# Kernel tuning notes

Measured on AMD Instinct MI355X. Metric: run time of the kernel, lower is better.

The kernel has to match this reference:

```python
import jax, jax.numpy as jnp
import numpy as np

NUM_CLASSES = 101
BATCH = 262144
LAMBDA = 1000.0


def setup_inputs() -> dict:
    key = jax.random.key(0)
    k1, k2 = jax.random.split(key)
    outputs = jax.random.normal(k1, (BATCH, NUM_CLASSES), dtype=jnp.float32)
    targets = jax.random.randint(k2, (BATCH,), 0, NUM_CLASSES, dtype=jnp.int64)
    return {"outputs": outputs, "targets": targets}


def reference(outputs, targets):
    B, C = outputs.shape
    targets = targets.reshape(-1)
    tf = targets.astype(outputs.dtype)

    probs = jax.nn.softmax(outputs, axis=1)                      # [B, C]
    labels = jnp.arange(C, dtype=outputs.dtype)                  # [C]
    pred_values = jnp.sum(probs * labels[None, :], axis=1)       # [B]
    centered = labels[None, :] - pred_values[:, None]            # [B, C]
    variance = jnp.sum(probs * centered * centered, axis=1)      # [B]
    variance = jnp.clip(variance, 1e-6, None)
    est_err = (pred_values - tf) ** 2
    concentrated_loss = jnp.mean(0.5 * jnp.log(variance) + est_err / (2.0 * variance))

    # Unimodal ordinal penalty, vectorized over the original double loop:
    # sign_j = -1 if j < target else +1; penalty = relu(-(p_j - p_{j+1}) * sign_j)
    j = jnp.arange(C - 1)                                        # [C-1]
    sign = jnp.where(j[None, :] < targets[:, None], -1.0, 1.0).astype(outputs.dtype)
    prob_diff = probs[:, :-1] - probs[:, 1:]                     # [B, C-1]
    penalty = jax.nn.relu(-prob_diff * sign)
    unimodal_loss = jnp.sum(penalty) / B
    weighted_unimodal_loss = LAMBDA * unimodal_loss

    total_loss = concentrated_loss + weighted_unimodal_loss
    return (total_loss, concentrated_loss, weighted_unimodal_loss)
```

## Files before the change

### kernel.cpp

```cpp
#include <hip/hip_runtime.h>
#include <hip/hip_bf16.h>


#define ROWS_PER_BLOCK 128
#define NCLASSES 101
#define LAMBDA_W 1000.0

__global__ __launch_bounds__(ROWS_PER_BLOCK)
void ucl_row_kernel(const float* __restrict__ x,
                    const int* __restrict__ tgt,
                    double* __restrict__ acc)
{
    __shared__ float lds[ROWS_PER_BLOCK * NCLASSES];

    const int tid = threadIdx.x;
    const int bid = blockIdx.x;

    {
        const float4* __restrict__ g4 =
            reinterpret_cast<const float4*>(x + (size_t)bid * (ROWS_PER_BLOCK * NCLASSES));
        float4* __restrict__ l4 = reinterpret_cast<float4*>(lds);
#pragma unroll
        for (int k = 0; k < 25; ++k)
            l4[tid + 128 * k] = g4[tid + 128 * k];
        if (tid < 32)
            l4[tid + 3200] = g4[tid + 3200];
    }
    __syncthreads();

    const float* __restrict__ xr = lds + tid * NCLASSES;
    const int t = tgt[(size_t)bid * ROWS_PER_BLOCK + tid];

    float S, W, Q, pen, eprev;
    {
        float e = __expf(xr[0]);
        S = e; W = 0.0f; Q = 0.0f; pen = 0.0f; eprev = e;
    }
#pragma unroll
    for (int j = 1; j < NCLASSES; ++j) {
        float e  = __expf(xr[j]);
        float fj = (float)j;
        S += e;
        W  = fmaf(e, fj, W);
        Q  = fmaf(e, fj * fj, Q);
        float d = eprev - e;
        float r = ((j - 1) < t) ? d : -d;
        pen += fmaxf(r, 0.0f);
        eprev = e;
    }

    const float pred = W / S;
    float var = fmaf(-pred, pred, Q / S);
    var = fmaxf(var, 1e-6f);
    const float err  = pred - (float)t;
    float conc = 0.5f * __logf(var) + err * err / (2.0f * var);
    float pens = pen / S;

#pragma unroll
    for (int off = 32; off > 0; off >>= 1) {
        conc += __shfl_down(conc, off);
        pens += __shfl_down(pens, off);
    }
    __syncthreads();
    if ((tid & 63) == 0) {
        lds[(tid >> 6) * 2 + 0] = conc;
        lds[(tid >> 6) * 2 + 1] = pens;
    }
    __syncthreads();
    if (tid == 0) {
        double c = (double)lds[0] + (double)lds[2];
        double p = (double)lds[1] + (double)lds[3];
        atomicAdd(&acc[0], c);
        atomicAdd(&acc[1], p);
    }
}

__global__ void ucl_finalize_kernel(const double* __restrict__ acc,
                                    float* __restrict__ out,
                                    double invB)
{
    double conc = acc[0] * invB;
    double uni  = acc[1] * invB * LAMBDA_W;
    out[0] = (float)(conc + uni);
    out[1] = (float)conc;
    out[2] = (float)uni;
}

extern "C" void kernel_launch(void* const* d_in, const int* in_sizes, int n_in,
                              void* d_out, int out_size, void* d_ws, size_t ws_size,
                              hipStream_t stream)
{
    const float* x   = (const float*)d_in[0];
    const int*   tgt = (const int*)d_in[1];
    float* out  = (float*)d_out;
    double* acc = (double*)d_ws;

    const int B = in_sizes[1];
    const int blocks = B / ROWS_PER_BLOCK;

    hipMemsetAsync(d_ws, 0, 2 * sizeof(double), stream);
    hipLaunchKernelGGL(ucl_row_kernel, dim3(blocks), dim3(ROWS_PER_BLOCK), 0, stream,
                       x, tgt, acc);
    hipLaunchKernelGGL(ucl_finalize_kernel, dim3(1), dim3(1), 0, stream,
                       acc, out, 1.0 / (double)B);
}
```

Before: 189.0 us.

## Split each row across two threads and replace atomics with per-block partials

Each block now uses 256 threads for 128 rows. The two halves of the class dimension are processed by separate threads and merged through shared memory, which doubles the parallelism available per row and shortens the serial exp chain. The global load is reorganized to issue all loads into registers before storing to LDS. When enough workspace is available, double atomics are replaced by per-block float2 partials summed in a tree-reducing finalize kernel, which also removes the memset. The cost is an extra barrier and some LDS traffic.

New measurement: 157.4 us. -16.7%, faster.

```diff
diff --git a/kernel.cpp b/kernel.cpp
--- a/kernel.cpp
+++ b/kernel.cpp
@@ -1,89 +1,156 @@
 #include <hip/hip_runtime.h>
-#include <hip/hip_bf16.h>
 
 
-#define ROWS_PER_BLOCK 128
-#define NCLASSES 101
+#define NR 128
+#define NT 256
+#define NC 101
 #define LAMBDA_W 1000.0
 
-__global__ __launch_bounds__(ROWS_PER_BLOCK)
+__global__ __launch_bounds__(NT, 3)
 void ucl_row_kernel(const float* __restrict__ x,
                     const int* __restrict__ tgt,
-                    double* __restrict__ acc)
+                    float2* __restrict__ partial,
+                    double* __restrict__ acc,
+                    int use_atomic)
 {
-    __shared__ float lds[ROWS_PER_BLOCK * NCLASSES];
+    __shared__ float tile[NR * NC];
+    __shared__ float part[NR * 4];
+    __shared__ float red[8];
 
     const int tid = threadIdx.x;
     const int bid = blockIdx.x;
 
     {
         const float4* __restrict__ g4 =
-            reinterpret_cast<const float4*>(x + (size_t)bid * (ROWS_PER_BLOCK * NCLASSES));
-        float4* __restrict__ l4 = reinterpret_cast<float4*>(lds);
+            reinterpret_cast<const float4*>(x + (size_t)bid * (NR * NC));
+        float4* __restrict__ l4 = reinterpret_cast<float4*>(tile);
+        float4 v[12]; float4 vt;
 #pragma unroll
-        for (int k = 0; k < 25; ++k)
-            l4[tid + 128 * k] = g4[tid + 128 * k];
-        if (tid < 32)
-            l4[tid + 3200] = g4[tid + 3200];
+        for (int k = 0; k < 12; ++k) v[k] = g4[tid + NT * k];
+        if (tid < 160) vt = g4[3072 + tid];
+#pragma unroll
+        for (int k = 0; k < 12; ++k) l4[tid + NT * k] = v[k];
+        if (tid < 160) l4[3072 + tid] = vt;
+    }
+
+    const int row = tid & (NR - 1);
+    const int t = tgt[(size_t)bid * NR + row];
+    __syncthreads();
+
+    const float* __restrict__ xr = tile + row * NC;
+    float S, W, Q, pen;
+    if (tid < NR) {
+        float e = __expf(xr[0]);
+        S = e; W = 0.f; Q = 0.f; pen = 0.f;
+        float eprev = e;
+#pragma unroll
+        for (int j = 1; j <= 50; ++j) {
+            float e2 = __expf(xr[j]);
+            float fj = (float)j;
+            S += e2;
+            W = fmaf(e2, fj, W);
+            Q = fmaf(e2, fj * fj, Q);
+            float d = eprev - e2;
+            float r = ((j - 1) < t) ? d : -d;
+            pen += fmaxf(r, 0.f);
+            eprev = e2;
+        }
+    } else {
+        float eprev = __expf(xr[50]);
+        S = 0.f; W = 0.f; Q = 0.f; pen = 0.f;
+#pragma unroll
+        for (int j = 51; j < NC; ++j) {
+            float e2 = __expf(xr[j]);
+            float fj = (float)j;
+            S += e2;
+            W = fmaf(e2, fj, W);
+            Q = fmaf(e2, fj * fj, Q);
+            float d = eprev - e2;
+            float r = ((j - 1) < t) ? d : -d;
+            pen += fmaxf(r, 0.f);
+            eprev = e2;
+        }
+        part[row * 4 + 0] = S;
+        part[row * 4 + 1] = W;
+        part[row * 4 + 2] = Q;
+        part[row * 4 + 3] = pen;
     }
     __syncthreads();
 
-    const float* __restrict__ xr = lds + tid * NCLASSES;
-    const int t = tgt[(size_t)bid * ROWS_PER_BLOCK + tid];
-
-    float S, W, Q, pen, eprev;
-    {
-        float e = __expf(xr[0]);
-        S = e; W = 0.0f; Q = 0.0f; pen = 0.0f; eprev = e;
+    float conc = 0.f, pens = 0.f;
+    if (tid < NR) {
+        S   += part[row * 4 + 0];
+        W   += part[row * 4 + 1];
+        Q   += part[row * 4 + 2];
+        pen += part[row * 4 + 3];
+        float pred = W / S;
+        float var = fmaf(-pred, pred, Q / S);
+        var = fmaxf(var, 1e-6f);
+        float err = pred - (float)t;
+        conc = 0.5f * __logf(var) + err * err / (2.0f * var);
+        pens = pen / S;
     }
-#pragma unroll
-    for (int j = 1; j < NCLASSES; ++j) {
-        float e  = __expf(xr[j]);
-        float fj = (float)j;
-        S += e;
-        W  = fmaf(e, fj, W);
-        Q  = fmaf(e, fj * fj, Q);
-        float d = eprev - e;
-        float r = ((j - 1) < t) ? d : -d;
-        pen += fmaxf(r, 0.0f);
-        eprev = e;
-    }
-
-    const float pred = W / S;
-    float var = fmaf(-pred, pred, Q / S);
-    var = fmaxf(var, 1e-6f);
-    const float err  = pred - (float)t;
-    float conc = 0.5f * __logf(var) + err * err / (2.0f * var);
-    float pens = pen / S;
 
 #pragma unroll
     for (int off = 32; off > 0; off >>= 1) {
         conc += __shfl_down(conc, off);
         pens += __shfl_down(pens, off);
     }
-    __syncthreads();
     if ((tid & 63) == 0) {
-        lds[(tid >> 6) * 2 + 0] = conc;
-        lds[(tid >> 6) * 2 + 1] = pens;
+        red[(tid >> 6) * 2 + 0] = conc;
+        red[(tid >> 6) * 2 + 1] = pens;
     }
     __syncthreads();
     if (tid == 0) {
-        double c = (double)lds[0] + (double)lds[2];
-        double p = (double)lds[1] + (double)lds[3];
-        atomicAdd(&acc[0], c);
-        atomicAdd(&acc[1], p);
+        float c = red[0] + red[2] + red[4] + red[6];
+        float p = red[1] + red[3] + red[5] + red[7];
+        if (use_atomic) {
+            atomicAdd(&acc[0], (double)c);
+            atomicAdd(&acc[1], (double)p);
+        } else {
+            partial[bid] = make_float2(c, p);
+        }
     }
 }
 
-__global__ void ucl_finalize_kernel(const double* __restrict__ acc,
-                                    float* __restrict__ out,
-                                    double invB)
+__global__ __launch_bounds__(256)
+void ucl_finalize(const float2* __restrict__ partial,
+                  const double* __restrict__ acc,
+                  float* __restrict__ out,
+                  int nblocks, double invB, int use_atomic)
 {
-    double conc = acc[0] * invB;
-    double uni  = acc[1] * invB * LAMBDA_W;
-    out[0] = (float)(conc + uni);
-    out[1] = (float)conc;
-    out[2] = (float)uni;
+    const int tid = threadIdx.x;
+    if (use_atomic) {
+        if (tid == 0) {
+            double C = acc[0] * invB;
+            double P = acc[1] * invB * LAMBDA_W;
+            out[0] = (float)(C + P);
+            out[1] = (float)C;
+            out[2] = (float)P;
+        }
+        return;
+    }
+    double c = 0.0, p = 0.0;
+    for (int i = tid; i < nblocks; i += 256) {
+        float2 v = partial[i];
+        c += (double)v.x;
+        p += (double)v.y;
+    }
+#pragma unroll
+    for (int off = 32; off > 0; off >>= 1) {
+        c += __shfl_down(c, off);
+        p += __shfl_down(p, off);
+    }
+    __shared__ double s[8];
+    if ((tid & 63) == 0) { s[(tid >> 6) * 2] = c; s[(tid >> 6) * 2 + 1] = p; }
+    __syncthreads();
+    if (tid == 0) {
+        double C = (s[0] + s[2] + s[4] + s[6]) * invB;
+        double P = (s[1] + s[3] + s[5] + s[7]) * invB * LAMBDA_W;
+        out[0] = (float)(C + P);
+        out[1] = (float)C;
+        out[2] = (float)P;
+    }
 }
 
 extern "C" void kernel_launch(void* const* d_in, const int* in_sizes, int n_in,
@@ -92,15 +159,21 @@
 {
     const float* x   = (const float*)d_in[0];
     const int*   tgt = (const int*)d_in[1];
-    float* out  = (float*)d_out;
+    float* out = (float*)d_out;
+
+    const int B = in_sizes[1];
+    const int blocks = B / NR;
+
+    const size_t need = (size_t)blocks * sizeof(float2);
+    const int use_atomic = (ws_size < need + 2 * sizeof(double)) ? 1 : 0;
+    float2* partial = (float2*)((char*)d_ws + 2 * sizeof(double));
     double* acc = (double*)d_ws;
 
-    const int B = in_sizes[1];
-    const int blocks = B / ROWS_PER_BLOCK;
+    if (use_atomic)
+        hipMemsetAsync(d_ws, 0, 2 * sizeof(double), stream);
 
-    hipMemsetAsync(d_ws, 0, 2 * sizeof(double), stream);
-    hipLaunchKernelGGL(ucl_row_kernel, dim3(blocks), dim3(ROWS_PER_BLOCK), 0, stream,
-                       x, tgt, acc);
-    hipLaunchKernelGGL(ucl_finalize_kernel, dim3(1), dim3(1), 0, stream,
-                       acc, out, 1.0 / (double)B);
+    hipLaunchKernelGGL(ucl_row_kernel, dim3(blocks), dim3(NT), 0, stream,
+                       x, tgt, partial, acc, use_atomic);
+    hipLaunchKernelGGL(ucl_finalize, dim3(1), dim3(256), 0, stream,
+                       partial, acc, out, blocks, 1.0 / (double)B, use_atomic);
 }
```

## Persistent double-buffered row kernel with async global-to-LDS loads and partial sums

Applied to the files above, without the earlier changes.

Turns the row kernel into a persistent kernel. At most 512 blocks each walk a contiguous range of 128-row tiles, and the next tile is prefetched into a second LDS buffer with global_load_lds while the current tile is computed. The double-precision atomics and the memset are replaced by per-block float2 partials, which a 256-thread finalize kernel reduces in double. The aim is to hide global load latency behind the exp/accumulate work and to drop the atomic and memset overhead. In exchange, the two ~52KB LDS buffers limit each CU to one 2-wave block, and correctness depends on the compiler's wait counts covering the async LDS writes.

New measurement: 173.9 us. 8.0% less time.

```diff
diff --git a/kernel.cpp b/kernel.cpp
--- a/kernel.cpp
+++ b/kernel.cpp
@@ -1,89 +1,132 @@
 #include <hip/hip_runtime.h>
-#include <hip/hip_bf16.h>
 
 
-#define ROWS_PER_BLOCK 128
-#define NCLASSES 101
+#define NT 128
+#define TR 128
+#define NC 101
+#define TILE_F4 3232
+#define PAD_F4 3328
+#define NBLK 512
 #define LAMBDA_W 1000.0
 
-__global__ __launch_bounds__(ROWS_PER_BLOCK)
+__device__ __forceinline__ void gload_lds16(const float4* g, float4* l)
+{
+    __builtin_amdgcn_global_load_lds(
+        (const __attribute__((address_space(1))) void*)g,
+        (__attribute__((address_space(3))) void*)l,
+        16, 0, 0);
+}
+
+__device__ __forceinline__ void prefetch_tile(const float4* __restrict__ g4,
+                                              float4* l4, int tid)
+{
+#pragma unroll
+    for (int k = 0; k < 25; ++k)
+        gload_lds16(g4 + k * NT + tid, l4 + k * NT + tid);
+    if (tid < 32)
+        gload_lds16(g4 + 25 * NT + tid, l4 + 25 * NT + tid);
+}
+
+__global__ __launch_bounds__(NT)
 void ucl_row_kernel(const float* __restrict__ x,
                     const int* __restrict__ tgt,
-                    double* __restrict__ acc)
+                    float2* __restrict__ partial,
+                    int ntiles)
 {
-    __shared__ float lds[ROWS_PER_BLOCK * NCLASSES];
+    __shared__ __align__(16) float4 buf[2][PAD_F4];
+    __shared__ float red[4];
 
     const int tid = threadIdx.x;
     const int bid = blockIdx.x;
+    const int nb  = gridDim.x;
 
-    {
-        const float4* __restrict__ g4 =
-            reinterpret_cast<const float4*>(x + (size_t)bid * (ROWS_PER_BLOCK * NCLASSES));
-        float4* __restrict__ l4 = reinterpret_cast<float4*>(lds);
+    const int tpb   = ntiles / nb;
+    const int rem   = ntiles - tpb * nb;
+    const int start = bid * tpb + (bid < rem ? bid : rem);
+    const int cnt   = tpb + (bid < rem ? 1 : 0);
+
+    const float4* __restrict__ x4 = (const float4*)x;
+
+    int t_cur = tgt[(size_t)start * TR + tid];
+    prefetch_tile(x4 + (size_t)start * TILE_F4, buf[0], tid);
+
+    float conc = 0.f, pens = 0.f;
+
+    for (int i = 0; i < cnt; ++i) {
+        __syncthreads();
+
+        if (i + 1 < cnt)
+            prefetch_tile(x4 + (size_t)(start + i + 1) * TILE_F4,
+                          buf[(i + 1) & 1], tid);
+        int t_next = (i + 1 < cnt) ? tgt[(size_t)(start + i + 1) * TR + tid] : 0;
+
+        const float* __restrict__ xr = (const float*)buf[i & 1] + tid * NC;
+        const int t = t_cur;
+
+        float e = __expf(xr[0]);
+        float S = e, W = 0.f, Q = 0.f, pen = 0.f, ep = e;
 #pragma unroll
-        for (int k = 0; k < 25; ++k)
-            l4[tid + 128 * k] = g4[tid + 128 * k];
-        if (tid < 32)
-            l4[tid + 3200] = g4[tid + 3200];
+        for (int j = 1; j < NC; ++j) {
+            float e2 = __expf(xr[j]);
+            float fj = (float)j;
+            S += e2;
+            W = fmaf(e2, fj, W);
+            Q = fmaf(e2, fj * fj, Q);
+            float d = ep - e2;
+            float r = ((j - 1) < t) ? d : -d;
+            pen += fmaxf(r, 0.f);
+            ep = e2;
+        }
+        float pred = W / S;
+        float var  = fmaxf(fmaf(-pred, pred, Q / S), 1e-6f);
+        float err  = pred - (float)t;
+        conc += 0.5f * __logf(var) + err * err / (2.0f * var);
+        pens += pen / S;
+
+        t_cur = t_next;
     }
-    __syncthreads();
-
-    const float* __restrict__ xr = lds + tid * NCLASSES;
-    const int t = tgt[(size_t)bid * ROWS_PER_BLOCK + tid];
-
-    float S, W, Q, pen, eprev;
-    {
-        float e = __expf(xr[0]);
-        S = e; W = 0.0f; Q = 0.0f; pen = 0.0f; eprev = e;
-    }
-#pragma unroll
-    for (int j = 1; j < NCLASSES; ++j) {
-        float e  = __expf(xr[j]);
-        float fj = (float)j;
-        S += e;
-        W  = fmaf(e, fj, W);
-        Q  = fmaf(e, fj * fj, Q);
-        float d = eprev - e;
-        float r = ((j - 1) < t) ? d : -d;
-        pen += fmaxf(r, 0.0f);
-        eprev = e;
-    }
-
-    const float pred = W / S;
-    float var = fmaf(-pred, pred, Q / S);
-    var = fmaxf(var, 1e-6f);
-    const float err  = pred - (float)t;
-    float conc = 0.5f * __logf(var) + err * err / (2.0f * var);
-    float pens = pen / S;
 
 #pragma unroll
     for (int off = 32; off > 0; off >>= 1) {
         conc += __shfl_down(conc, off);
         pens += __shfl_down(pens, off);
     }
-    __syncthreads();
     if ((tid & 63) == 0) {
-        lds[(tid >> 6) * 2 + 0] = conc;
-        lds[(tid >> 6) * 2 + 1] = pens;
+        red[(tid >> 6) * 2 + 0] = conc;
+        red[(tid >> 6) * 2 + 1] = pens;
     }
     __syncthreads();
-    if (tid == 0) {
-        double c = (double)lds[0] + (double)lds[2];
-        double p = (double)lds[1] + (double)lds[3];
-        atomicAdd(&acc[0], c);
-        atomicAdd(&acc[1], p);
-    }
+    if (tid == 0)
+        partial[bid] = make_float2(red[0] + red[2], red[1] + red[3]);
 }
 
-__global__ void ucl_finalize_kernel(const double* __restrict__ acc,
-                                    float* __restrict__ out,
-                                    double invB)
+__global__ __launch_bounds__(256)
+void ucl_finalize(const float2* __restrict__ partial,
+                  float* __restrict__ out,
+                  int nblocks, double invB)
 {
-    double conc = acc[0] * invB;
-    double uni  = acc[1] * invB * LAMBDA_W;
-    out[0] = (float)(conc + uni);
-    out[1] = (float)conc;
-    out[2] = (float)uni;
+    const int tid = threadIdx.x;
+    double c = 0.0, p = 0.0;
+    for (int i = tid; i < nblocks; i += 256) {
+        float2 v = partial[i];
+        c += (double)v.x;
+        p += (double)v.y;
+    }
+#pragma unroll
+    for (int off = 32; off > 0; off >>= 1) {
+        c += __shfl_down(c, off);
+        p += __shfl_down(p, off);
+    }
+    __shared__ double s[8];
+    if ((tid & 63) == 0) { s[(tid >> 6) * 2] = c; s[(tid >> 6) * 2 + 1] = p; }
+    __syncthreads();
+    if (tid == 0) {
+        double C = (s[0] + s[2] + s[4] + s[6]) * invB;
+        double P = (s[1] + s[3] + s[5] + s[7]) * invB * LAMBDA_W;
+        out[0] = (float)(C + P);
+        out[1] = (float)C;
+        out[2] = (float)P;
+    }
 }
 
 extern "C" void kernel_launch(void* const* d_in, const int* in_sizes, int n_in,
@@ -92,15 +135,15 @@
 {
     const float* x   = (const float*)d_in[0];
     const int*   tgt = (const int*)d_in[1];
-    float* out  = (float*)d_out;
-    double* acc = (double*)d_ws;
+    float* out = (float*)d_out;
+    float2* partial = (float2*)d_ws;
 
     const int B = in_sizes[1];
-    const int blocks = B / ROWS_PER_BLOCK;
+    const int ntiles = B / TR;
+    const int blocks = (ntiles < NBLK) ? ntiles : NBLK;
 
-    hipMemsetAsync(d_ws, 0, 2 * sizeof(double), stream);
-    hipLaunchKernelGGL(ucl_row_kernel, dim3(blocks), dim3(ROWS_PER_BLOCK), 0, stream,
-                       x, tgt, acc);
-    hipLaunchKernelGGL(ucl_finalize_kernel, dim3(1), dim3(1), 0, stream,
-                       acc, out, 1.0 / (double)B);
+    hipLaunchKernelGGL(ucl_row_kernel, dim3(blocks), dim3(NT), 0, stream,
+                       x, tgt, partial, ntiles);
+    hipLaunchKernelGGL(ucl_finalize, dim3(1), dim3(256), 0, stream,
+                       partial, out, blocks, 1.0 / (double)B);
 }
```
